# Kernel tuning notes

Measured on AMD Instinct MI355X. Metric: run time of the kernel, lower is better.

## Reference

```python
import jax, jax.numpy as jnp
import numpy as np

B, L, C = 4, 2048, 512
H, D = 8, 512          # n_head, hidden_dim (per-head dim)
TEMP = 1.0
EPS = 1e-5


def setup_inputs() -> dict:
    key = jax.random.key(0)
    ks = jax.random.split(key, 12)
    s_in = 1.0 / np.sqrt(C)
    s_out = 1.0 / np.sqrt(H * D)
    return {
        "q": jax.random.normal(ks[0], (B, L, C), jnp.float32),
        "k": jax.random.normal(ks[1], (B, L, C), jnp.float32),
        "v": jax.random.normal(ks[2], (B, L, C), jnp.float32),
        "mask": jax.random.randint(ks[3], (B, L, L), 0, 2).astype(bool),
        "Wq": jax.random.normal(ks[4], (C, H * D), jnp.float32) * s_in,
        "bq": jnp.zeros((H * D,), jnp.float32),
        "Wk": jax.random.normal(ks[5], (C, H * D), jnp.float32) * s_in,
        "bk": jnp.zeros((H * D,), jnp.float32),
        "Wv": jax.random.normal(ks[6], (C, H * D), jnp.float32) * s_in,
        "bv": jnp.zeros((H * D,), jnp.float32),
        "Wo": jax.random.normal(ks[7], (H * D, D), jnp.float32) * s_out,
        "bo": jnp.zeros((D,), jnp.float32),
        "gamma": jnp.ones((D,), jnp.float32),
        "beta": jnp.zeros((D,), jnp.float32),
    }


def reference(q, k, v, mask, Wq, bq, Wk, bk, Wv, bv, Wo, bo, gamma, beta):
    b, ql, _ = q.shape
    residual = q
    qh = (q @ Wq + bq).reshape(b, ql, H, D)           # b,l,h,d
    kh = (k @ Wk + bk).reshape(b, ql, H, D)
    vh = (v @ Wv + bv).reshape(b, ql, H, D)
    # scores in head-major layout to mirror torch permute(2,0,1,3)
    scores = jnp.einsum("bqhd,bkhd->hbqk", qh, kh) / TEMP  # h,b,l,l
    scores = jnp.where(mask[None], -jnp.inf, scores)
    atten = jax.nn.softmax(scores, axis=-1)                 # h,b,l,l
    ctx = jnp.einsum("hbqk,bkhd->bqhd", atten, vh)          # b,l,h,d
    ctx = ctx.reshape(b, ql, H * D)
    out = ctx @ Wo + bo                                     # b,l,D  (dropout in eval mode)
    x = out + residual
    mu = jnp.mean(x, axis=-1, keepdims=True)
    var = jnp.var(x, axis=-1, keepdims=True)
    out = (x - mu) / jnp.sqrt(var + EPS) * gamma + beta
    return out, atten.reshape(H * b, ql, ql)
```

## Files before the change

kernel.cpp:

```cpp
#include <hip/hip_runtime.h>
#include <stdint.h>


typedef unsigned short u16;
typedef _Float16 f16;
typedef __attribute__((ext_vector_type(4))) _Float16 f16x4;
typedef __attribute__((ext_vector_type(8))) _Float16 f16x8;
typedef __attribute__((ext_vector_type(4))) float f32x4;

#define EPI_QKH    0
#define EPI_VHT    1
#define EPI_SCORES 2
#define EPI_CTX    3
#define EPI_OUT    4

__device__ __forceinline__ f32x4 mfma16(f16x8 a, f16x8 b, f32x4 c) {
  return __builtin_amdgcn_mfma_f32_16x16x32_f16(a, b, c, 0, 0, 0);
}

__device__ __forceinline__ void stage_tile_f16(const char* gbase, size_t grow, char* lds, int tid) {
  const int lane = tid & 63, wave = tid >> 6;
#pragma unroll
  for (int c = 0; c < 2; ++c) {
    int chunk = wave * 2 + c;
    int off = chunk * 1024 + lane * 16;
    int r = off >> 6;
    int cb = off & 63;
    const char* g = gbase + (size_t)r * grow + cb;
    __builtin_amdgcn_global_load_lds(
        (__attribute__((address_space(1))) void*)g,
        (__attribute__((address_space(3))) void*)(lds + chunk * 1024),
        16, 0, 0);
  }
}

__device__ __forceinline__ f16x8 load_frag16(const char* lds, int row, int kq) {
  return *(const f16x8*)(lds + ((size_t)row * 32 + kq) * 2);
}

template<int EPI>
__global__ __launch_bounds__(256, 2)
void gemm_k(const char* __restrict__ A, const char* __restrict__ B,
            int lda, int ldb, int K,
            char* __restrict__ C0,
            const float* __restrict__ bias, const float* __restrict__ resid) {
  __shared__ alignas(16) char smem[3 * 16384];

  const int tid = threadIdx.x, lane = tid & 63, wave = tid >> 6;
  const int wm = wave >> 1, wn = wave & 1;

  const int nx = gridDim.x, ny = gridDim.y;
  int id = blockIdx.x + nx * blockIdx.y;
  const int chunk = (nx * ny) >> 3;
  id = (id & 7) * chunk + (id >> 3);
  const int m0 = (id % nx) * 128, n0 = (id / nx) * 128;

  const char* pA = A; const char* pB = B;
  int kz = 0;
  if constexpr (EPI == EPI_SCORES) {
    int z = blockIdx.z, h = z >> 2, b = z & 3;
    size_t e2 = ((size_t)b * 2048 * 4096 + (size_t)h * 512) * 2;
    pA += e2; pB += e2;
  } else if constexpr (EPI == EPI_CTX) {
    int z = blockIdx.z, h = z >> 2, b = z & 3;
    pA += ((size_t)z << 22) * 2;
    pB += ((size_t)(b * 8 + h) * 512 * 2048) * 2;
  } else if constexpr (EPI == EPI_OUT) {
    kz = blockIdx.z;
    pA += (size_t)kz * 2048 * 2;
    pB += (size_t)kz * 2048 * 2;
  }

  f32x4 acc[4][4];
#pragma unroll
  for (int i = 0; i < 4; ++i)
#pragma unroll
    for (int j = 0; j < 4; ++j) acc[i][j] = (f32x4){0.f, 0.f, 0.f, 0.f};

  const size_t rowA = (size_t)lda * 2, rowB = (size_t)ldb * 2;
  const char* gA = pA + (size_t)m0 * rowA;
  const char* gB = pB + (size_t)n0 * rowB;

  const int nk = K >> 5;
  const int kq = (lane >> 4) * 8, l15 = lane & 15, quad = lane >> 4;

  stage_tile_f16(gA, rowA, smem, tid);
  stage_tile_f16(gB, rowB, smem + 8192, tid);
  stage_tile_f16(gA + 64, rowA, smem + 16384, tid);
  stage_tile_f16(gB + 64, rowB, smem + 16384 + 8192, tid);

  int bc = 0;
  for (int kt = 0; kt < nk; ++kt) {
    if (kt + 1 < nk) { asm volatile("s_waitcnt vmcnt(4)" ::: "memory"); }
    else             { asm volatile("s_waitcnt vmcnt(0)" ::: "memory"); }
    __builtin_amdgcn_sched_barrier(0);
    __builtin_amdgcn_s_barrier();
    __builtin_amdgcn_sched_barrier(0);

    if (kt + 2 < nk) {
      int b2 = bc + 2; if (b2 >= 3) b2 -= 3;
      char* nb = smem + b2 * 16384;
      stage_tile_f16(gA + (size_t)(kt + 2) * 64, rowA, nb, tid);
      stage_tile_f16(gB + (size_t)(kt + 2) * 64, rowB, nb + 8192, tid);
    }

    char* cur = smem + bc * 16384;
    f16x8 af[4], bf[4];
#pragma unroll
    for (int mi = 0; mi < 4; ++mi)
      af[mi] = load_frag16(cur, wm * 64 + mi * 16 + l15, kq);
#pragma unroll
    for (int ni = 0; ni < 4; ++ni)
      bf[ni] = load_frag16(cur + 8192, wn * 64 + ni * 16 + l15, kq);

    __builtin_amdgcn_s_setprio(1);
#pragma unroll
    for (int mi = 0; mi < 4; ++mi)
#pragma unroll
      for (int ni = 0; ni < 4; ++ni)
        acc[mi][ni] = mfma16(af[mi], bf[ni], acc[mi][ni]);
    __builtin_amdgcn_s_setprio(0);

    bc = (bc + 1 == 3) ? 0 : bc + 1;
  }

#pragma unroll
  for (int mi = 0; mi < 4; ++mi)
#pragma unroll
    for (int ni = 0; ni < 4; ++ni)
#pragma unroll
      for (int r = 0; r < 4; ++r) {
        int m = m0 + wm * 64 + mi * 16 + quad * 4 + r;
        int n = n0 + wn * 64 + ni * 16 + l15;
        float v = acc[mi][ni][r];
        if constexpr (EPI == EPI_QKH) {
          v += bias[n];
          ((f16*)C0)[(size_t)m * 4096 + n] = (f16)v;
        } else if constexpr (EPI == EPI_VHT) {
          v += bias[m];
          int hh = m >> 9, d = m & 511, bb = n >> 11, ll = n & 2047;
          ((f16*)C0)[(((size_t)(bb * 8 + hh) * 512 + d) << 11) + ll] = (f16)v;
        } else if constexpr (EPI == EPI_SCORES) {
          int z = blockIdx.z;
          ((float*)C0)[((size_t)z << 22) + ((size_t)m << 11) + n] = v;
        } else if constexpr (EPI == EPI_CTX) {
          int z = blockIdx.z, hh = z >> 2, bb = z & 3;
          ((f16*)C0)[((size_t)(bb * 2048 + m) << 12) + hh * 512 + n] = (f16)v;
        } else {
          if (kz == 0) v += bias[n] + resid[((size_t)m << 9) + n];
          ((float*)C0)[(size_t)kz * 8192 * 512 + ((size_t)m << 9) + n] = v;
        }
      }
}

__global__ __launch_bounds__(256)
void transpose_cvt_k(const float* __restrict__ in, f16* __restrict__ T,
                     int R, int Cc) {
  __shared__ f16 tile[32][33];
  const int t = threadIdx.x, tc = t & 31, tr = t >> 5;
  const int bx = blockIdx.x, by = blockIdx.y;
#pragma unroll
  for (int k = 0; k < 4; ++k) {
    int r = by * 32 + tr + k * 8;
    tile[tr + k * 8][tc] = (f16)in[(size_t)r * Cc + bx * 32 + tc];
  }
  __syncthreads();
#pragma unroll
  for (int k = 0; k < 4; ++k) {
    int c = bx * 32 + tr + k * 8;
    T[(size_t)c * R + by * 32 + tc] = tile[tc][tr + k * 8];
  }
}

__global__ __launch_bounds__(256)
void cvt_f16_k(const float* __restrict__ in, f16* __restrict__ out) {
  int i = blockIdx.x * 256 + threadIdx.x;
  float4 v = ((const float4*)in)[i];
  f16x4 h;
  h[0] = (f16)v.x; h[1] = (f16)v.y; h[2] = (f16)v.z; h[3] = (f16)v.w;
  ((f16x4*)out)[i] = h;
}

__global__ __launch_bounds__(256)
void maskprep_k(const int* __restrict__ m32, unsigned char* __restrict__ m8) {
  int i = blockIdx.x * 256 + threadIdx.x;
  int4 v = ((const int4*)m32)[i];
  uchar4 c;
  c.x = (unsigned char)v.x; c.y = (unsigned char)v.y;
  c.z = (unsigned char)v.z; c.w = (unsigned char)v.w;
  ((uchar4*)m8)[i] = c;
}

__global__ __launch_bounds__(256)
void softmax_k(float* __restrict__ att, const unsigned char* __restrict__ m8,
               f16* __restrict__ att16) {
  __shared__ float sm[4];
  int t = threadIdx.x, lane = t & 63, wave = t >> 6;
  size_t r = blockIdx.x;
  int z = (int)(r >> 11), m = (int)(r & 2047), b = z & 3;
  float4* row = (float4*)(att + (r << 11));
  const uchar4* mrow = (const uchar4*)(m8 + (((size_t)b << 22) + ((size_t)m << 11)));
  float4 a = row[t], c = row[t + 256];
  uchar4 ma = mrow[t], mc = mrow[t + 256];
  if (ma.x) a.x = -1e30f; if (ma.y) a.y = -1e30f;
  if (ma.z) a.z = -1e30f; if (ma.w) a.w = -1e30f;
  if (mc.x) c.x = -1e30f; if (mc.y) c.y = -1e30f;
  if (mc.z) c.z = -1e30f; if (mc.w) c.w = -1e30f;
  float mx = fmaxf(fmaxf(fmaxf(a.x, a.y), fmaxf(a.z, a.w)),
                   fmaxf(fmaxf(c.x, c.y), fmaxf(c.z, c.w)));
#pragma unroll
  for (int o = 32; o > 0; o >>= 1) mx = fmaxf(mx, __shfl_xor(mx, o));
  if (lane == 0) sm[wave] = mx;
  __syncthreads();
  mx = fmaxf(fmaxf(sm[0], sm[1]), fmaxf(sm[2], sm[3]));
  a.x = __expf(a.x - mx); a.y = __expf(a.y - mx);
  a.z = __expf(a.z - mx); a.w = __expf(a.w - mx);
  c.x = __expf(c.x - mx); c.y = __expf(c.y - mx);
  c.z = __expf(c.z - mx); c.w = __expf(c.w - mx);
  float s = a.x + a.y + a.z + a.w + c.x + c.y + c.z + c.w;
#pragma unroll
  for (int o = 32; o > 0; o >>= 1) s += __shfl_xor(s, o);
  __syncthreads();
  if (lane == 0) sm[wave] = s;
  __syncthreads();
  s = sm[0] + sm[1] + sm[2] + sm[3];
  float inv = 1.0f / s;
  a.x *= inv; a.y *= inv; a.z *= inv; a.w *= inv;
  c.x *= inv; c.y *= inv; c.z *= inv; c.w *= inv;
  row[t] = a; row[t + 256] = c;
  f16x4* r16 = (f16x4*)(att16 + (r << 11));
  f16x4 ha, hc;
  ha[0] = (f16)a.x; ha[1] = (f16)a.y; ha[2] = (f16)a.z; ha[3] = (f16)a.w;
  hc[0] = (f16)c.x; hc[1] = (f16)c.y; hc[2] = (f16)c.z; hc[3] = (f16)c.w;
  r16[t] = ha; r16[t + 256] = hc;
}

__global__ __launch_bounds__(256)
void ln_k(const float* __restrict__ x0, const float* __restrict__ x1,
          const float* __restrict__ gamma, const float* __restrict__ beta,
          float* __restrict__ out) {
  __shared__ float s1[4], s2[4];
  int t = threadIdx.x, lane = t & 63, wave = t >> 6;
  size_t base = (size_t)blockIdx.x << 9;
  float2 va = ((const float2*)(x0 + base))[t];
  float2 vb = ((const float2*)(x1 + base))[t];
  float2 v; v.x = va.x + vb.x; v.y = va.y + vb.y;
  float s = v.x + v.y;
  float q = v.x * v.x + v.y * v.y;
#pragma unroll
  for (int o = 32; o > 0; o >>= 1) { s += __shfl_xor(s, o); q += __shfl_xor(q, o); }
  if (lane == 0) { s1[wave] = s; s2[wave] = q; }
  __syncthreads();
  s = s1[0] + s1[1] + s1[2] + s1[3];
  q = s2[0] + s2[1] + s2[2] + s2[3];
  float mu = s * (1.0f / 512.0f);
  float var = q * (1.0f / 512.0f) - mu * mu;
  float rs = rsqrtf(var + 1e-5f);
  float2 g = ((const float2*)gamma)[t];
  float2 bb = ((const float2*)beta)[t];
  float2 o2;
  o2.x = (v.x - mu) * rs * g.x + bb.x;
  o2.y = (v.y - mu) * rs * g.y + bb.y;
  ((float2*)(out + base))[t] = o2;
}

extern "C" void kernel_launch(void* const* d_in, const int* in_sizes, int n_in,
                              void* d_out, int out_size, void* d_ws, size_t ws_size,
                              hipStream_t stream) {
  (void)in_sizes; (void)n_in; (void)out_size; (void)ws_size;
  const float* q     = (const float*)d_in[0];
  const float* k     = (const float*)d_in[1];
  const float* v     = (const float*)d_in[2];
  const int*   mask  = (const int*)d_in[3];
  const float* Wq    = (const float*)d_in[4];
  const float* bq    = (const float*)d_in[5];
  const float* Wk    = (const float*)d_in[6];
  const float* bk    = (const float*)d_in[7];
  const float* Wv    = (const float*)d_in[8];
  const float* bv    = (const float*)d_in[9];
  const float* Wo    = (const float*)d_in[10];
  const float* bo    = (const float*)d_in[11];
  const float* gamma = (const float*)d_in[12];
  const float* beta  = (const float*)d_in[13];

  float* out0  = (float*)d_out;
  float* atten = out0 + (size_t)4 * 2048 * 512;

  char* ws = (char*)d_ws;
  const size_t MB = 1024ull * 1024ull;
  f16* WqT  = (f16*)(ws + 0 * MB);
  f16* WkT  = (f16*)(ws + 4 * MB);
  f16* WvT  = (f16*)(ws + 8 * MB);
  f16* WoT  = (f16*)(ws + 12 * MB);
  unsigned char* mask8 = (unsigned char*)(ws + 16 * MB);
  f16* q16  = (f16*)(ws + 32 * MB);
  f16* k16  = (f16*)(ws + 40 * MB);
  f16* v16  = (f16*)(ws + 48 * MB);
  f16* vhT  = (f16*)(ws + 56 * MB);
  f16* atten16 = (f16*)(ws + 120 * MB);
  f16* qh   = (f16*)(ws + 120 * MB);
  f16* kh   = (f16*)(ws + 184 * MB);
  f16* ctx  = (f16*)(ws + 376 * MB);
  float* xbuf = (float*)(ws + 120 * MB);

  transpose_cvt_k<<<dim3(128, 16), 256, 0, stream>>>(Wq, WqT, 512, 4096);
  transpose_cvt_k<<<dim3(128, 16), 256, 0, stream>>>(Wk, WkT, 512, 4096);
  transpose_cvt_k<<<dim3(128, 16), 256, 0, stream>>>(Wv, WvT, 512, 4096);
  transpose_cvt_k<<<dim3(16, 128), 256, 0, stream>>>(Wo, WoT, 4096, 512);
  maskprep_k<<<16384, 256, 0, stream>>>(mask, mask8);
  cvt_f16_k<<<4096, 256, 0, stream>>>(q, q16);
  cvt_f16_k<<<4096, 256, 0, stream>>>(k, k16);
  cvt_f16_k<<<4096, 256, 0, stream>>>(v, v16);

  gemm_k<EPI_QKH><<<dim3(64, 32, 1), 256, 0, stream>>>(
      (const char*)q16, (const char*)WqT, 512, 512, 512, (char*)qh, bq, nullptr);
  gemm_k<EPI_QKH><<<dim3(64, 32, 1), 256, 0, stream>>>(
      (const char*)k16, (const char*)WkT, 512, 512, 512, (char*)kh, bk, nullptr);

  gemm_k<EPI_VHT><<<dim3(32, 64, 1), 256, 0, stream>>>(
      (const char*)WvT, (const char*)v16, 512, 512, 512, (char*)vhT, bv, nullptr);

  gemm_k<EPI_SCORES><<<dim3(16, 16, 32), 256, 0, stream>>>(
      (const char*)qh, (const char*)kh, 4096, 4096, 512, (char*)atten, nullptr, nullptr);

  softmax_k<<<65536, 256, 0, stream>>>(atten, mask8, atten16);

  gemm_k<EPI_CTX><<<dim3(16, 4, 32), 256, 0, stream>>>(
      (const char*)atten16, (const char*)vhT, 2048, 2048, 2048, (char*)ctx, nullptr, nullptr);

  gemm_k<EPI_OUT><<<dim3(64, 4, 2), 256, 0, stream>>>(
      (const char*)ctx, (const char*)WoT, 4096, 4096, 2048, (char*)xbuf, bo, q);

  ln_k<<<8192, 256, 0, stream>>>(xbuf, xbuf + (size_t)8192 * 512, gamma, beta, out0);
}
```

Measured before the change: 1.535 ms.

## Use 256x256 block tiles with 512 threads for projection, score and context GEMMs

Adds a gemm256_k variant that computes 256x256 output tiles with 8 waves. Each wave owns a 128x64 sub-tile with 32 accumulators, and the kernel keeps the triple-buffered global-to-LDS pipeline. The Q/K/V projections, the score GEMM and the context GEMM switch to it, while the split-K output GEMM stays on the old 128x128 kernel. The goal is higher arithmetic intensity and less global and LDS traffic per MFMA. In exchange it uses 96KB of LDS per block, which likely allows only one block per CU, raises register pressure, and leaves fewer blocks for the context GEMM.

```diff
diff --git a/kernel.cpp b/kernel.cpp
--- a/kernel.cpp
+++ b/kernel.cpp
@@ -39,24 +39,22 @@
 }
 
 template<int EPI>
-__global__ __launch_bounds__(256, 2)
-void gemm_k(const char* __restrict__ A, const char* __restrict__ B,
-            int lda, int ldb, int K,
-            char* __restrict__ C0,
-            const float* __restrict__ bias, const float* __restrict__ resid) {
-  __shared__ alignas(16) char smem[3 * 16384];
+__global__ __launch_bounds__(512, 2)
+void gemm256_k(const char* __restrict__ A, const char* __restrict__ B,
+               int lda, int ldb, int K,
+               char* __restrict__ C0, const float* __restrict__ bias) {
+  __shared__ alignas(16) char smem[3][32768];
 
   const int tid = threadIdx.x, lane = tid & 63, wave = tid >> 6;
-  const int wm = wave >> 1, wn = wave & 1;
+  const int wm = wave >> 2, wn = wave & 3;
 
   const int nx = gridDim.x, ny = gridDim.y;
   int id = blockIdx.x + nx * blockIdx.y;
   const int chunk = (nx * ny) >> 3;
   id = (id & 7) * chunk + (id >> 3);
-  const int m0 = (id % nx) * 128, n0 = (id / nx) * 128;
+  const int m0 = (id % nx) * 256, n0 = (id / nx) * 256;
 
   const char* pA = A; const char* pB = B;
-  int kz = 0;
   if constexpr (EPI == EPI_SCORES) {
     int z = blockIdx.z, h = z >> 2, b = z & 3;
     size_t e2 = ((size_t)b * 2048 * 4096 + (size_t)h * 512) * 2;
@@ -65,15 +63,11 @@
     int z = blockIdx.z, h = z >> 2, b = z & 3;
     pA += ((size_t)z << 22) * 2;
     pB += ((size_t)(b * 8 + h) * 512 * 2048) * 2;
-  } else if constexpr (EPI == EPI_OUT) {
-    kz = blockIdx.z;
-    pA += (size_t)kz * 2048 * 2;
-    pB += (size_t)kz * 2048 * 2;
-  }
-
-  f32x4 acc[4][4];
-#pragma unroll
-  for (int i = 0; i < 4; ++i)
+  }
+
+  f32x4 acc[8][4];
+#pragma unroll
+  for (int i = 0; i < 8; ++i)
 #pragma unroll
     for (int j = 0; j < 4; ++j) acc[i][j] = (f32x4){0.f, 0.f, 0.f, 0.f};
 
@@ -84,10 +78,10 @@
   const int nk = K >> 5;
   const int kq = (lane >> 4) * 8, l15 = lane & 15, quad = lane >> 4;
 
-  stage_tile_f16(gA, rowA, smem, tid);
-  stage_tile_f16(gB, rowB, smem + 8192, tid);
-  stage_tile_f16(gA + 64, rowA, smem + 16384, tid);
-  stage_tile_f16(gB + 64, rowB, smem + 16384 + 8192, tid);
+  stage_tile_f16(gA, rowA, smem[0], tid);
+  stage_tile_f16(gB, rowB, smem[0] + 16384, tid);
+  stage_tile_f16(gA + 64, rowA, smem[1], tid);
+  stage_tile_f16(gB + 64, rowB, smem[1] + 16384, tid);
 
   int bc = 0;
   for (int kt = 0; kt < nk; ++kt) {
@@ -99,23 +93,23 @@
 
     if (kt + 2 < nk) {
       int b2 = bc + 2; if (b2 >= 3) b2 -= 3;
-      char* nb = smem + b2 * 16384;
+      char* nb = smem[b2];
       stage_tile_f16(gA + (size_t)(kt + 2) * 64, rowA, nb, tid);
-      stage_tile_f16(gB + (size_t)(kt + 2) * 64, rowB, nb + 8192, tid);
+      stage_tile_f16(gB + (size_t)(kt + 2) * 64, rowB, nb + 16384, tid);
     }
 
-    char* cur = smem + bc * 16384;
-    f16x8 af[4], bf[4];
-#pragma unroll
-    for (int mi = 0; mi < 4; ++mi)
-      af[mi] = load_frag16(cur, wm * 64 + mi * 16 + l15, kq);
+    char* cur = smem[bc];
+    f16x8 af[8], bf[4];
+#pragma unroll
+    for (int mi = 0; mi < 8; ++mi)
+      af[mi] = load_frag16(cur, wm * 128 + mi * 16 + l15, kq);
 #pragma unroll
     for (int ni = 0; ni < 4; ++ni)
-      bf[ni] = load_frag16(cur + 8192, wn * 64 + ni * 16 + l15, kq);
+      bf[ni] = load_frag16(cur + 16384, wn * 64 + ni * 16 + l15, kq);
 
     __builtin_amdgcn_s_setprio(1);
 #pragma unroll
-    for (int mi = 0; mi < 4; ++mi)
+    for (int mi = 0; mi < 8; ++mi)
 #pragma unroll
       for (int ni = 0; ni < 4; ++ni)
         acc[mi][ni] = mfma16(af[mi], bf[ni], acc[mi][ni]);
@@ -125,12 +119,12 @@
   }
 
 #pragma unroll
-  for (int mi = 0; mi < 4; ++mi)
+  for (int mi = 0; mi < 8; ++mi)
 #pragma unroll
     for (int ni = 0; ni < 4; ++ni)
 #pragma unroll
       for (int r = 0; r < 4; ++r) {
-        int m = m0 + wm * 64 + mi * 16 + quad * 4 + r;
+        int m = m0 + wm * 128 + mi * 16 + quad * 4 + r;
         int n = n0 + wn * 64 + ni * 16 + l15;
         float v = acc[mi][ni][r];
         if constexpr (EPI == EPI_QKH) {
@@ -146,7 +140,98 @@
         } else if constexpr (EPI == EPI_CTX) {
           int z = blockIdx.z, hh = z >> 2, bb = z & 3;
           ((f16*)C0)[((size_t)(bb * 2048 + m) << 12) + hh * 512 + n] = (f16)v;
-        } else {
+        }
+      }
+}
+
+template<int EPI>
+__global__ __launch_bounds__(256, 2)
+void gemm_k(const char* __restrict__ A, const char* __restrict__ B,
+            int lda, int ldb, int K,
+            char* __restrict__ C0,
+            const float* __restrict__ bias, const float* __restrict__ resid) {
+  __shared__ alignas(16) char smem[3 * 16384];
+
+  const int tid = threadIdx.x, lane = tid & 63, wave = tid >> 6;
+  const int wm = wave >> 1, wn = wave & 1;
+
+  const int nx = gridDim.x, ny = gridDim.y;
+  int id = blockIdx.x + nx * blockIdx.y;
+  const int chunk = (nx * ny) >> 3;
+  id = (id & 7) * chunk + (id >> 3);
+  const int m0 = (id % nx) * 128, n0 = (id / nx) * 128;
+
+  const char* pA = A; const char* pB = B;
+  int kz = 0;
+  if constexpr (EPI == EPI_OUT) {
+    kz = blockIdx.z;
+    pA += (size_t)kz * 2048 * 2;
+    pB += (size_t)kz * 2048 * 2;
+  }
+
+  f32x4 acc[4][4];
+#pragma unroll
+  for (int i = 0; i < 4; ++i)
+#pragma unroll
+    for (int j = 0; j < 4; ++j) acc[i][j] = (f32x4){0.f, 0.f, 0.f, 0.f};
+
+  const size_t rowA = (size_t)lda * 2, rowB = (size_t)ldb * 2;
+  const char* gA = pA + (size_t)m0 * rowA;
+  const char* gB = pB + (size_t)n0 * rowB;
+
+  const int nk = K >> 5;
+  const int kq = (lane >> 4) * 8, l15 = lane & 15, quad = lane >> 4;
+
+  stage_tile_f16(gA, rowA, smem, tid);
+  stage_tile_f16(gB, rowB, smem + 8192, tid);
+  stage_tile_f16(gA + 64, rowA, smem + 16384, tid);
+  stage_tile_f16(gB + 64, rowB, smem + 16384 + 8192, tid);
+
+  int bc = 0;
+  for (int kt = 0; kt < nk; ++kt) {
+    if (kt + 1 < nk) { asm volatile("s_waitcnt vmcnt(4)" ::: "memory"); }
+    else             { asm volatile("s_waitcnt vmcnt(0)" ::: "memory"); }
+    __builtin_amdgcn_sched_barrier(0);
+    __builtin_amdgcn_s_barrier();
+    __builtin_amdgcn_sched_barrier(0);
+
+    if (kt + 2 < nk) {
+      int b2 = bc + 2; if (b2 >= 3) b2 -= 3;
+      char* nb = smem + b2 * 16384;
+      stage_tile_f16(gA + (size_t)(kt + 2) * 64, rowA, nb, tid);
+      stage_tile_f16(gB + (size_t)(kt + 2) * 64, rowB, nb + 8192, tid);
+    }
+
+    char* cur = smem + bc * 16384;
+    f16x8 af[4], bf[4];
+#pragma unroll
+    for (int mi = 0; mi < 4; ++mi)
+      af[mi] = load_frag16(cur, wm * 64 + mi * 16 + l15, kq);
+#pragma unroll
+    for (int ni = 0; ni < 4; ++ni)
+      bf[ni] = load_frag16(cur + 8192, wn * 64 + ni * 16 + l15, kq);
+
+    __builtin_amdgcn_s_setprio(1);
+#pragma unroll
+    for (int mi = 0; mi < 4; ++mi)
+#pragma unroll
+      for (int ni = 0; ni < 4; ++ni)
+        acc[mi][ni] = mfma16(af[mi], bf[ni], acc[mi][ni]);
+    __builtin_amdgcn_s_setprio(0);
+
+    bc = (bc + 1 == 3) ? 0 : bc + 1;
+  }
+
+#pragma unroll
+  for (int mi = 0; mi < 4; ++mi)
+#pragma unroll
+    for (int ni = 0; ni < 4; ++ni)
+#pragma unroll
+      for (int r = 0; r < 4; ++r) {
+        int m = m0 + wm * 64 + mi * 16 + quad * 4 + r;
+        int n = n0 + wn * 64 + ni * 16 + l15;
+        float v = acc[mi][ni][r];
+        if constexpr (EPI == EPI_OUT) {
           if (kz == 0) v += bias[n] + resid[((size_t)m << 9) + n];
           ((float*)C0)[(size_t)kz * 8192 * 512 + ((size_t)m << 9) + n] = v;
         }
@@ -312,21 +397,21 @@
   cvt_f16_k<<<4096, 256, 0, stream>>>(k, k16);
   cvt_f16_k<<<4096, 256, 0, stream>>>(v, v16);
 
-  gemm_k<EPI_QKH><<<dim3(64, 32, 1), 256, 0, stream>>>(
-      (const char*)q16, (const char*)WqT, 512, 512, 512, (char*)qh, bq, nullptr);
-  gemm_k<EPI_QKH><<<dim3(64, 32, 1), 256, 0, stream>>>(
-      (const char*)k16, (const char*)WkT, 512, 512, 512, (char*)kh, bk, nullptr);
-
-  gemm_k<EPI_VHT><<<dim3(32, 64, 1), 256, 0, stream>>>(
-      (const char*)WvT, (const char*)v16, 512, 512, 512, (char*)vhT, bv, nullptr);
-
-  gemm_k<EPI_SCORES><<<dim3(16, 16, 32), 256, 0, stream>>>(
-      (const char*)qh, (const char*)kh, 4096, 4096, 512, (char*)atten, nullptr, nullptr);
+  gemm256_k<EPI_QKH><<<dim3(32, 16, 1), 512, 0, stream>>>(
+      (const char*)q16, (const char*)WqT, 512, 512, 512, (char*)qh, bq);
+  gemm256_k<EPI_QKH><<<dim3(32, 16, 1), 512, 0, stream>>>(
+      (const char*)k16, (const char*)WkT, 512, 512, 512, (char*)kh, bk);
+
+  gemm256_k<EPI_VHT><<<dim3(16, 32, 1), 512, 0, stream>>>(
+      (const char*)WvT, (const char*)v16, 512, 512, 512, (char*)vhT, bv);
+
+  gemm256_k<EPI_SCORES><<<dim3(8, 8, 32), 512, 0, stream>>>(
+      (const char*)qh, (const char*)kh, 4096, 4096, 512, (char*)atten, nullptr);
 
   softmax_k<<<65536, 256, 0, stream>>>(atten, mask8, atten16);
 
-  gemm_k<EPI_CTX><<<dim3(16, 4, 32), 256, 0, stream>>>(
-      (const char*)atten16, (const char*)vhT, 2048, 2048, 2048, (char*)ctx, nullptr, nullptr);
+  gemm256_k<EPI_CTX><<<dim3(8, 2, 32), 512, 0, stream>>>(
+      (const char*)atten16, (const char*)vhT, 2048, 2048, 2048, (char*)ctx, nullptr);
 
   gemm_k<EPI_OUT><<<dim3(64, 4, 2), 256, 0, stream>>>(
       (const char*)ctx, (const char*)WoT, 4096, 4096, 2048, (char*)xbuf, bo, q);
```

Measured after the change: 1.495 ms. -2.6%, faster.
